# Optimization experiments

Measured on AMD Instinct MI355X. Metric: run time of the kernel, lower is better.

## Reference

```python
import jax, jax.numpy as jnp
import numpy as np

B, N, D = 4, 4096, 1024
H, S, R = 16, 256, 2           # heads, segment size, dilation rate
DH = D // H
LN_EPS = 1e-5


def _hilbert_perm(n_side):
    # perm[d] = linear index (y*side + x) of the d-th point on the Hilbert curve
    def d2xy(n, d):
        x = y = 0
        t = d
        s = 1
        while s < n:
            rx = 1 & (t // 2)
            ry = 1 & (t ^ rx)
            if ry == 0:
                if rx == 1:
                    x = s - 1 - x
                    y = s - 1 - y
                x, y = y, x
            x += s * rx
            y += s * ry
            t //= 4
            s *= 2
        return x, y
    perm = np.empty(n_side * n_side, dtype=np.int32)
    for d in range(n_side * n_side):
        xx, yy = d2xy(n_side, d)
        perm[d] = yy * n_side + xx
    return perm


def setup_inputs() -> dict:
    key = jax.random.key(0)
    ks = jax.random.split(key, 8)
    sc = 0.02
    return {
        "x": jax.random.normal(ks[0], (B, N, D), jnp.float32),
        "ln1_g": jnp.ones((D,), jnp.float32),
        "ln1_b": jnp.zeros((D,), jnp.float32),
        "w_qkv": jax.random.normal(ks[1], (D, 3 * D), jnp.float32) * sc,
        "b_qkv": jnp.zeros((3 * D,), jnp.float32),
        "w_o": jax.random.normal(ks[2], (D, D), jnp.float32) * sc,
        "b_o": jnp.zeros((D,), jnp.float32),
        "ln2_g": jnp.ones((D,), jnp.float32),
        "ln2_b": jnp.zeros((D,), jnp.float32),
        "w1": jax.random.normal(ks[3], (D, 4 * D), jnp.float32) * sc,
        "b1": jnp.zeros((4 * D,), jnp.float32),
        "w2": jax.random.normal(ks[4], (4 * D, D), jnp.float32) * sc,
        "b2": jnp.zeros((D,), jnp.float32),
        "hilbert_perm": jnp.asarray(_hilbert_perm(int(np.sqrt(N)))),
    }


def _layernorm(x, g, b):
    mu = jnp.mean(x, axis=-1, keepdims=True)
    var = jnp.mean(jnp.square(x - mu), axis=-1, keepdims=True)
    return (x - mu) * jax.lax.rsqrt(var + LN_EPS) * g + b


def _hilbert_dilated_attention(x, w_qkv, b_qkv, w_o, b_o, perm):
    b, n, d = x.shape
    nseg, sr = n // S, S // R
    xp = jnp.take(x, perm, axis=1)                    # Hilbert reorder
    qkv = xp @ w_qkv + b_qkv                          # [b,n,3d]
    q, k, v = jnp.split(qkv, 3, axis=-1)
    def seg(t):
        return t.reshape(b, nseg, S, H, DH)
    q, k, v = seg(q), seg(k), seg(v)
    # per-head dilation offset: head h attends positions (h % R) :: R in each segment
    offs = jnp.arange(H, dtype=jnp.int32) % R                        # [H]
    idx = offs[None, :] + R * jnp.arange(sr, dtype=jnp.int32)[:, None]  # [sr,H]
    idx_g = idx[None, None, :, :, None]                              # [1,1,sr,H,1]
    qd = jnp.take_along_axis(q, idx_g, axis=2)        # [b,nseg,sr,H,dh]
    kd = jnp.take_along_axis(k, idx_g, axis=2)
    vd = jnp.take_along_axis(v, idx_g, axis=2)
    scores = jnp.einsum('bgqhd,bgkhd->bghqk', qd, kd) / jnp.sqrt(jnp.asarray(DH, x.dtype))
    attn = jax.nn.softmax(scores, axis=-1)
    od = jnp.einsum('bghqk,bgkhd->bgqhd', attn, vd)   # [b,nseg,sr,H,dh]
    # scatter back into full segments; uncovered (head,pos) slots stay zero
    out = jnp.zeros((b, nseg, S, H, DH), x.dtype)
    out = out.at[:, :, idx, jnp.arange(H)[None, :], :].set(od)
    out = out.reshape(b, n, d) @ w_o + b_o
    inv = jnp.argsort(perm)
    return jnp.take(out, inv, axis=1)                 # inverse Hilbert reorder


def reference(x, ln1_g, ln1_b, w_qkv, b_qkv, w_o, b_o, ln2_g, ln2_b, w1, b1, w2, b2, hilbert_perm):
    h = _layernorm(x, ln1_g, ln1_b)
    h = _hilbert_dilated_attention(h, w_qkv, b_qkv, w_o, b_o, hilbert_perm)
    x = x + h
    h = _layernorm(x, ln2_g, ln2_b)
    h = jax.nn.gelu(h @ w1 + b1, approximate=False) @ w2 + b2
    return x + h
```

## Files before the change

kernel.cpp:

```cpp
#include <hip/hip_runtime.h>

typedef short bf16x8 __attribute__((ext_vector_type(8)));
typedef float f32x4 __attribute__((ext_vector_type(4)));
typedef unsigned short u16;

#define GLDS16(g, l) __builtin_amdgcn_global_load_lds( \
    (const __attribute__((address_space(1))) void*)(g), \
    (__attribute__((address_space(3))) void*)(l), 16, 0, 0)

#define DSR_(dst, p) asm volatile("ds_read_b128 %0, %1" \
    : "=v"(dst) : "v"((const __attribute__((address_space(3))) void*)(p)))

__device__ __forceinline__ u16 f2b(float f) {
  unsigned u = __float_as_uint(f);
  u += 0x7fffu + ((u >> 16) & 1u);
  return (u16)(u >> 16);
}

__global__ __launch_bounds__(256)
void transpose_bf16(const float* __restrict__ w, u16* __restrict__ wt, int K, int N) {
  __shared__ float tile[32][33];
  const int n0 = blockIdx.x * 32, k0 = blockIdx.y * 32;
  const int tx = threadIdx.x & 31, ty = threadIdx.x >> 5;
#pragma unroll
  for (int i = 0; i < 4; ++i)
    tile[ty + i * 8][tx] = w[(size_t)(k0 + ty + i * 8) * N + n0 + tx];
  __syncthreads();
#pragma unroll
  for (int i = 0; i < 4; ++i)
    wt[(size_t)(n0 + ty + i * 8) * K + k0 + tx] = f2b(tile[tx][ty + i * 8]);
}

__global__ __launch_bounds__(256)
void transpose_qkv_pack(const float* __restrict__ w, u16* __restrict__ wp) {
  __shared__ float tile[32][33];
  const int n0 = blockIdx.x * 32, k0 = blockIdx.y * 32;
  const int tx = threadIdx.x & 31, ty = threadIdx.x >> 5;
#pragma unroll
  for (int i = 0; i < 4; ++i)
    tile[ty + i * 8][tx] = w[(size_t)(k0 + ty + i * 8) * 3072 + n0 + tx];
  __syncthreads();
#pragma unroll
  for (int i = 0; i < 4; ++i) {
    const int col = n0 + ty + i * 8;
    const int q = (col >> 6) & 1;
    const int np = (col >> 10) * 512 + ((col >> 7) & 7) * 64 + (col & 63);
    wp[(size_t)q * (1536 * 1024) + (size_t)np * 1024 + k0 + tx] = f2b(tile[tx][ty + i * 8]);
  }
}

__global__ __launch_bounds__(256)
void transpose_wo_pack(const float* __restrict__ w, u16* __restrict__ wp) {
  __shared__ float tile[32][33];
  const int n0 = blockIdx.x * 32, k0 = blockIdx.y * 32;
  const int tx = threadIdx.x & 31, ty = threadIdx.x >> 5;
#pragma unroll
  for (int i = 0; i < 4; ++i)
    tile[ty + i * 8][tx] = w[(size_t)(k0 + ty + i * 8) * 1024 + n0 + tx];
  __syncthreads();
#pragma unroll
  for (int i = 0; i < 4; ++i) {
    const int n = n0 + ty + i * 8;
    const int k = k0 + tx;
    const int q = (k >> 6) & 1;
    const int kp = (k >> 7) * 64 + (k & 63);
    wp[(size_t)q * (1024 * 512) + (size_t)n * 512 + kp] = f2b(tile[tx][ty + i * 8]);
  }
}

__global__ __launch_bounds__(256)
void ln_rows(const float* __restrict__ src, const float* __restrict__ gam,
             const float* __restrict__ bet, const int* __restrict__ perm,
             u16* __restrict__ dst) {
  const int orow = blockIdx.x;
  const int b = orow >> 12, j = orow & 4095;
  const int srow = perm ? ((b << 12) + perm[j]) : orow;
  const float4 v = ((const float4*)(src + (size_t)srow * 1024))[threadIdx.x];
  float s = v.x + v.y + v.z + v.w;
  float s2 = v.x * v.x + v.y * v.y + v.z * v.z + v.w * v.w;
#pragma unroll
  for (int d = 1; d < 64; d <<= 1) { s += __shfl_xor(s, d); s2 += __shfl_xor(s2, d); }
  __shared__ float rs[4], rs2[4];
  const int wave = threadIdx.x >> 6, lane = threadIdx.x & 63;
  if (lane == 0) { rs[wave] = s; rs2[wave] = s2; }
  __syncthreads();
  s = rs[0] + rs[1] + rs[2] + rs[3];
  s2 = rs2[0] + rs2[1] + rs2[2] + rs2[3];
  const float mu = s * (1.f / 1024.f);
  const float var = s2 * (1.f / 1024.f) - mu * mu;
  const float rstd = rsqrtf(var + 1e-5f);
  const int c = threadIdx.x * 4;
  const float4 gg = *(const float4*)(gam + c);
  const float4 bb = *(const float4*)(bet + c);
  const u16 o0 = f2b((v.x - mu) * rstd * gg.x + bb.x);
  const u16 o1 = f2b((v.y - mu) * rstd * gg.y + bb.y);
  const u16 o2 = f2b((v.z - mu) * rstd * gg.z + bb.z);
  const u16 o3 = f2b((v.w - mu) * rstd * gg.w + bb.w);
  const unsigned lo = (unsigned)o0 | ((unsigned)o1 << 16);
  const unsigned hi = (unsigned)o2 | ((unsigned)o3 << 16);
  *(uint2*)(dst + (size_t)orow * 1024 + c) = make_uint2(lo, hi);
}

template <int EPI, int PAR>
__global__ __launch_bounds__(512, 2)
void gemm256(const u16* __restrict__ A, const u16* __restrict__ Bt,
             const float* __restrict__ bias, void* __restrict__ Cout,
             const float* __restrict__ resid, const int* __restrict__ perm,
             int M, int Nn, int K, int aRS,
             long aParOff, long bParOff, long cParOff) {
  __shared__ u16 sm[65536];
  char* const smc = (char*)sm;
  const int tid = threadIdx.x;
  const int w = tid >> 6, lane = tid & 63;
  const int lr = lane & 15, lg = lane >> 4;
  const int wm = w >> 2, wn = w & 3;

  int wg = blockIdx.x;
  int par = 0;
  if (PAR) { par = wg & 1; wg >>= 1; }
  const int x = wg & 7, l = wg >> 3;
  const int band = (M >> 8) >> 3;
  const int mm = l % band, nn = l / band;
  const int m0 = (x * band + mm) << 8;
  const int n0 = nn << 8;

  const int srow = tid >> 3;
  const int scol = ((tid & 7) ^ (srow & 7)) << 3;
  const size_t aSrc = (size_t)(m0 + srow) * aRS + (PAR ? (size_t)par * aParOff : 0) + scol;
  const size_t bSrc = (size_t)(n0 + srow) * K + (PAR ? (size_t)par * bParOff : 0) + scol;
  char* const lWav = smc + w * 1024;

  const int slot0 = (lg ^ (lr & 7)) << 4;
  const int aRow = (wm * 128 + lr) * 128;
  const int bRow = (wn * 64 + lr) * 128 + 32768;

  const int NT = K >> 6;

#define STAGE_(d, mat, h, k0) do { \
    const size_t rs_ = (mat) ? (size_t)K : (size_t)aRS; \
    const u16* gp = ((mat) ? Bt : A) + ((mat) ? bSrc : aSrc) + (size_t)(h) * 128 * rs_ + (k0); \
    char* lp = lWav + (d) * 65536 + (mat) * 32768 + (h) * 16384; \
    GLDS16(gp, lp); GLDS16(gp + 64 * rs_, lp + 8192); } while (0)

  bf16x8 aLo[8], aHi[8], bLo[4], bHi[4];

#define R_ALO(P) do { _Pragma("unroll") for (int mf = 0; mf < 4; ++mf) \
    _Pragma("unroll") for (int kk = 0; kk < 2; ++kk) \
      DSR_(aLo[mf * 2 + kk], (P) + mf * 2048 + (slot0 ^ (kk << 6))); } while (0)
#define R_AHI(P) do { _Pragma("unroll") for (int mf = 0; mf < 4; ++mf) \
    _Pragma("unroll") for (int kk = 0; kk < 2; ++kk) \
      DSR_(aHi[mf * 2 + kk], (P) + (4 + mf) * 2048 + (slot0 ^ (kk << 6))); } while (0)
#define R_BLO(P) do { _Pragma("unroll") for (int nf = 0; nf < 2; ++nf) \
    _Pragma("unroll") for (int kk = 0; kk < 2; ++kk) \
      DSR_(bLo[nf * 2 + kk], (P) + nf * 2048 + (slot0 ^ (kk << 6))); } while (0)
#define R_BHI(P) do { _Pragma("unroll") for (int nf = 0; nf < 2; ++nf) \
    _Pragma("unroll") for (int kk = 0; kk < 2; ++kk) \
      DSR_(bHi[nf * 2 + kk], (P) + (2 + nf) * 2048 + (slot0 ^ (kk << 6))); } while (0)

#define QUAD_(AARR, BARR, MB, NB) do { _Pragma("unroll") for (int mf = 0; mf < 4; ++mf) \
    _Pragma("unroll") for (int nf = 0; nf < 2; ++nf) \
    _Pragma("unroll") for (int kk = 0; kk < 2; ++kk) \
      acc[(MB) * 4 + mf][(NB) * 2 + nf] = __builtin_amdgcn_mfma_f32_16x16x32_bf16( \
          AARR[mf * 2 + kk], BARR[nf * 2 + kk], acc[(MB) * 4 + mf][(NB) * 2 + nf], 0, 0, 0); } while (0)

#define LGKM0SB_() do { asm volatile("s_waitcnt lgkmcnt(0)" ::: "memory"); \
                        __builtin_amdgcn_sched_barrier(0); } while (0)

  STAGE_(0, 1, 0, 0); STAGE_(0, 1, 1, 0); STAGE_(0, 0, 0, 0); STAGE_(0, 0, 1, 0);
  if (NT > 1) {
    STAGE_(1, 1, 0, 64); STAGE_(1, 1, 1, 64); STAGE_(1, 0, 0, 64); STAGE_(1, 0, 1, 64);
    asm volatile("s_waitcnt vmcnt(8)" ::: "memory");
  } else {
    asm volatile("s_waitcnt vmcnt(0)" ::: "memory");
  }
  __builtin_amdgcn_s_barrier();

  f32x4 acc[8][4] = {};

  for (int t = 0; t < NT; ++t) {
    const int c = t & 1;
    const char* cA = smc + c * 65536 + aRow;
    const char* cB = smc + c * 65536 + bRow;
    const int k2 = (t + 2) << 6;

    R_ALO(cA); R_BLO(cB);
    LGKM0SB_();
    __builtin_amdgcn_s_setprio(1);
    QUAD_(aLo, bLo, 0, 0);
    __builtin_amdgcn_s_setprio(0);
    R_BHI(cB);
    LGKM0SB_();
    __builtin_amdgcn_s_setprio(1);
    QUAD_(aLo, bHi, 0, 1);
    __builtin_amdgcn_s_setprio(0);
    __builtin_amdgcn_s_barrier();

    if (t + 2 < NT) { STAGE_(c, 1, 0, k2); STAGE_(c, 1, 1, k2); }
    R_AHI(cA);
    LGKM0SB_();
    __builtin_amdgcn_s_setprio(1);
    QUAD_(aHi, bLo, 1, 0);
    __builtin_amdgcn_s_setprio(0);
    __builtin_amdgcn_s_barrier();

    if (t + 2 < NT) { STAGE_(c, 0, 0, k2); STAGE_(c, 0, 1, k2); }
    __builtin_amdgcn_s_setprio(1);
    QUAD_(aHi, bHi, 1, 1);
    __builtin_amdgcn_s_setprio(0);
    if (t < NT - 2) asm volatile("s_waitcnt vmcnt(8)" ::: "memory");
    else            asm volatile("s_waitcnt vmcnt(0)" ::: "memory");
    __builtin_amdgcn_s_barrier();
  }
#undef STAGE_
#undef R_ALO
#undef R_AHI
#undef R_BLO
#undef R_BHI
#undef QUAD_
#undef LGKM0SB_

#pragma unroll
  for (int mf = 0; mf < 8; ++mf) {
#pragma unroll
    for (int nf = 0; nf < 4; ++nf) {
      const int col = n0 + wn * 64 + nf * 16 + lr;
      float bia;
      if (PAR && EPI == 0) {
        const int s = col >> 9, hh2 = (col >> 6) & 7, d = col & 63;
        bia = bias[s * 1024 + hh2 * 128 + par * 64 + d];
      } else {
        bia = bias[col];
      }
#pragma unroll
      for (int r = 0; r < 4; ++r) {
        const int row = m0 + wm * 128 + mf * 16 + lg * 4 + r;
        float v = acc[mf][nf][r] + bia;
        if (EPI == 0) {
          ((u16*)Cout)[(PAR ? (size_t)par * cParOff : 0) + (size_t)row * Nn + col] = f2b(v);
        } else if (EPI == 1) {
          v = 0.5f * v * (1.f + erff(v * 0.70710678118654752f));
          ((u16*)Cout)[(size_t)row * Nn + col] = f2b(v);
        } else if (EPI == 2) {
          const int orig = PAR ? (2 * row + par) : row;
          const int b2 = orig >> 12, jj = orig & 4095;
          const size_t di = ((size_t)((b2 << 12) + perm[jj])) * 1024 + col;
          ((float*)Cout)[di] = resid[di] + v;
        } else {
          const size_t di = (size_t)row * 1024 + col;
          ((float*)Cout)[di] = resid[di] + v;
        }
      }
    }
  }
}

__global__ __launch_bounds__(256, 2)
void attn_kernel(const u16* __restrict__ qkvp, u16* __restrict__ op) {
  const int blk = blockIdx.x;
  const int h = blk & 15, g = (blk >> 4) & 15, b = blk >> 8;
  const int tid = threadIdx.x, wave = tid >> 6, lane = tid & 63;
  const int lr = lane & 15, lg = lane >> 4;
  const int par = h & 1, hh = h >> 1;

  __shared__ u16 lQ[128 * 64];
  __shared__ u16 lK[128 * 64];
  __shared__ u16 lVt[64 * 128];
  __shared__ u16 lP[4][32 * 128];

  const u16* qp = qkvp + (size_t)par * (8192 * 1536);
  u16* opb = op + (size_t)par * (8192 * 512);
  const int rbase = (b << 11) + (g << 7);

#pragma unroll
  for (int i = 0; i < 4; ++i) {
    const int ou = i * 4096 + wave * 1024;
    const int o = ou + lane * 16;
    const int j = o >> 7, cb = o & 127;
    const u16* gq = qp + (size_t)(rbase + j) * 1536 + hh * 64 + (cb >> 1);
    GLDS16(gq, (char*)lQ + ou);
    GLDS16(gq + 512, (char*)lK + ou);
  }
#pragma unroll
  for (int i = 0; i < 4; ++i) {
    const int c = tid + i * 256;
    const int j = c >> 3, dc = c & 7;
    const uint4 vv = *(const uint4*)(qp + (size_t)(rbase + j) * 1536 + 1024 + hh * 64 + dc * 8);
    const u16* pv = (const u16*)&vv;
#pragma unroll
    for (int e = 0; e < 8; ++e) lVt[(dc * 8 + e) * 128 + j] = pv[e];
  }
  __syncthreads();

  f32x4 sacc[2][8] = {};
#pragma unroll
  for (int kk = 0; kk < 2; ++kk) {
    bf16x8 aq[2], bk[8];
#pragma unroll
    for (int mf = 0; mf < 2; ++mf)
      aq[mf] = *(const bf16x8*)&lQ[(wave * 32 + mf * 16 + lr) * 64 + kk * 32 + lg * 8];
#pragma unroll
    for (int nf = 0; nf < 8; ++nf)
      bk[nf] = *(const bf16x8*)&lK[(nf * 16 + lr) * 64 + kk * 32 + lg * 8];
#pragma unroll
    for (int mf = 0; mf < 2; ++mf)
#pragma unroll
      for (int nf = 0; nf < 8; ++nf)
        sacc[mf][nf] = __builtin_amdgcn_mfma_f32_16x16x32_bf16(aq[mf], bk[nf], sacc[mf][nf], 0, 0, 0);
  }

#pragma unroll
  for (int mf = 0; mf < 2; ++mf) {
#pragma unroll
    for (int r = 0; r < 4; ++r) {
      float mx = -3e38f;
#pragma unroll
      for (int nf = 0; nf < 8; ++nf) mx = fmaxf(mx, sacc[mf][nf][r]);
#pragma unroll
      for (int d = 1; d < 16; d <<= 1) mx = fmaxf(mx, __shfl_xor(mx, d));
      float pv[8];
      float sum = 0.f;
#pragma unroll
      for (int nf = 0; nf < 8; ++nf) {
        pv[nf] = __expf((sacc[mf][nf][r] - mx) * 0.125f);
        sum += pv[nf];
      }
#pragma unroll
      for (int d = 1; d < 16; d <<= 1) sum += __shfl_xor(sum, d);
      const float inv = 1.f / sum;
      const int rrow = mf * 16 + lg * 4 + r;
#pragma unroll
      for (int nf = 0; nf < 8; ++nf)
        lP[wave][rrow * 128 + nf * 16 + lr] = f2b(pv[nf] * inv);
    }
  }
  __syncthreads();

  f32x4 oacc[2][4] = {};
#pragma unroll
  for (int kk = 0; kk < 4; ++kk) {
    bf16x8 ap[2], bv[4];
#pragma unroll
    for (int mf = 0; mf < 2; ++mf)
      ap[mf] = *(const bf16x8*)&lP[wave][(mf * 16 + lr) * 128 + kk * 32 + lg * 8];
#pragma unroll
    for (int nf = 0; nf < 4; ++nf)
      bv[nf] = *(const bf16x8*)&lVt[(nf * 16 + lr) * 128 + kk * 32 + lg * 8];
#pragma unroll
    for (int mf = 0; mf < 2; ++mf)
#pragma unroll
      for (int nf = 0; nf < 4; ++nf)
        oacc[mf][nf] = __builtin_amdgcn_mfma_f32_16x16x32_bf16(ap[mf], bv[nf], oacc[mf][nf], 0, 0, 0);
  }

  u16* obase = opb + (size_t)rbase * 512 + hh * 64;
#pragma unroll
  for (int mf = 0; mf < 2; ++mf)
#pragma unroll
    for (int nf = 0; nf < 4; ++nf)
#pragma unroll
      for (int r = 0; r < 4; ++r) {
        const int jq = wave * 32 + mf * 16 + lg * 4 + r;
        obase[(size_t)jq * 512 + nf * 16 + lr] = f2b(oacc[mf][nf][r]);
      }
}

extern "C" void kernel_launch(void* const* d_in, const int* in_sizes, int n_in,
                              void* d_out, int out_size, void* d_ws, size_t ws_size,
                              hipStream_t stream) {
  const float* x    = (const float*)d_in[0];
  const float* ln1g = (const float*)d_in[1];
  const float* ln1b = (const float*)d_in[2];
  const float* wqkv = (const float*)d_in[3];
  const float* bqkv = (const float*)d_in[4];
  const float* wo   = (const float*)d_in[5];
  const float* bo   = (const float*)d_in[6];
  const float* ln2g = (const float*)d_in[7];
  const float* ln2b = (const float*)d_in[8];
  const float* w1   = (const float*)d_in[9];
  const float* b1   = (const float*)d_in[10];
  const float* w2   = (const float*)d_in[11];
  const float* b2   = (const float*)d_in[12];
  const int*   perm = (const int*)d_in[13];
  float* out = (float*)d_out;
  char* ws = (char*)d_ws;

  u16*  r0    = (u16*)ws;
  u16*  qkvp  = (u16*)(ws + (32ull << 20));
  u16*  op    = (u16*)(ws + (80ull << 20));
  u16*  a1    = (u16*)(ws + (32ull << 20));
  float* x2   = (float*)(ws + (160ull << 20));
  u16*  wqkvP = (u16*)(ws + (224ull << 20));
  u16*  woP   = (u16*)(ws + (230ull << 20));
  u16*  w1T   = (u16*)(ws + (232ull << 20));
  u16*  w2T   = (u16*)(ws + (240ull << 20));

  transpose_qkv_pack<<<dim3(96, 32), 256, 0, stream>>>(wqkv, wqkvP);
  transpose_wo_pack<<<dim3(32, 32), 256, 0, stream>>>(wo, woP);
  transpose_bf16<<<dim3(4096 / 32, 1024 / 32), 256, 0, stream>>>(w1, w1T, 1024, 4096);
  transpose_bf16<<<dim3(1024 / 32, 4096 / 32), 256, 0, stream>>>(w2, w2T, 4096, 1024);

  ln_rows<<<16384, 256, 0, stream>>>(x, ln1g, ln1b, perm, r0);
  gemm256<0, 1><<<384, 512, 0, stream>>>(r0, wqkvP, bqkv, qkvp, nullptr, nullptr,
                                         8192, 1536, 1024, 2048,
                                         1024L, 1536L * 1024, 8192L * 1536);
  attn_kernel<<<1024, 256, 0, stream>>>(qkvp, op);
  gemm256<2, 1><<<256, 512, 0, stream>>>(op, woP, bo, x2, x, perm,
                                         8192, 1024, 512, 512,
                                         8192L * 512, 1024L * 512, 0);
  ln_rows<<<16384, 256, 0, stream>>>(x2, ln2g, ln2b, nullptr, r0);
  gemm256<1, 0><<<1024, 512, 0, stream>>>(r0, w1T, b1, a1, nullptr, nullptr,
                                          16384, 4096, 1024, 1024, 0, 0, 0);
  gemm256<3, 0><<<256, 512, 0, stream>>>(a1, w2T, b2, out, x2, nullptr,
                                         16384, 1024, 4096, 4096, 0, 0, 0);
}
```

Before: 531.2 us.

## Switch GEMM to 256x128 tiles with triple-buffered LDS pipeline

The GEMM tile shrinks from 256x256 to 256x128, doubling the grid for every projection. The ping-pong double buffer with staged half-tile loads and four barriers per k-step becomes a three-slot ring buffer: each step loads all of A and B fragments, issues the next-next prefetch, then runs a single MFMA block with one barrier. The aim is fewer barriers per step, more workgroups to fill the CUs, and fewer accumulator registers. The cost is lower arithmetic intensity per tile, with more A reloads from global memory, and less overlap between LDS reads and MFMA work.

Measured after the change: 572.7 us. 1.08x slower.

```diff
diff --git a/kernel.cpp b/kernel.cpp
--- a/kernel.cpp
+++ b/kernel.cpp
@@ -108,7 +108,7 @@
              const float* __restrict__ resid, const int* __restrict__ perm,
              int M, int Nn, int K, int aRS,
              long aParOff, long bParOff, long cParOff) {
-  __shared__ u16 sm[65536];
+  __shared__ u16 sm[3 * 24576];
   char* const smc = (char*)sm;
   const int tid = threadIdx.x;
   const int w = tid >> 6, lane = tid & 63;
@@ -122,108 +122,80 @@
   const int band = (M >> 8) >> 3;
   const int mm = l % band, nn = l / band;
   const int m0 = (x * band + mm) << 8;
-  const int n0 = nn << 8;
+  const int n0 = nn << 7;
 
   const int srow = tid >> 3;
   const int scol = ((tid & 7) ^ (srow & 7)) << 3;
   const size_t aSrc = (size_t)(m0 + srow) * aRS + (PAR ? (size_t)par * aParOff : 0) + scol;
   const size_t bSrc = (size_t)(n0 + srow) * K + (PAR ? (size_t)par * bParOff : 0) + scol;
-  char* const lWav = smc + w * 1024;
 
   const int slot0 = (lg ^ (lr & 7)) << 4;
   const int aRow = (wm * 128 + lr) * 128;
-  const int bRow = (wn * 64 + lr) * 128 + 32768;
+  const int bRow = 32768 + (wn * 32 + lr) * 128;
 
   const int NT = K >> 6;
 
-#define STAGE_(d, mat, h, k0) do { \
-    const size_t rs_ = (mat) ? (size_t)K : (size_t)aRS; \
-    const u16* gp = ((mat) ? Bt : A) + ((mat) ? bSrc : aSrc) + (size_t)(h) * 128 * rs_ + (k0); \
-    char* lp = lWav + (d) * 65536 + (mat) * 32768 + (h) * 16384; \
-    GLDS16(gp, lp); GLDS16(gp + 64 * rs_, lp + 8192); } while (0)
-
-  bf16x8 aLo[8], aHi[8], bLo[4], bHi[4];
-
-#define R_ALO(P) do { _Pragma("unroll") for (int mf = 0; mf < 4; ++mf) \
+#define STAGE_T(d, k0) do { \
+    _Pragma("unroll") for (int i = 0; i < 4; ++i) \
+      GLDS16(A + aSrc + (size_t)(64 * i) * aRS + (k0), smc + (d) * 49152 + w * 1024 + i * 8192); \
+    _Pragma("unroll") for (int i = 0; i < 2; ++i) \
+      GLDS16(Bt + bSrc + (size_t)(64 * i) * K + (k0), smc + (d) * 49152 + 32768 + w * 1024 + i * 8192); \
+  } while (0)
+
+  bf16x8 a[16], b[4];
+
+#define R_A(P) do { _Pragma("unroll") for (int mf = 0; mf < 8; ++mf) \
     _Pragma("unroll") for (int kk = 0; kk < 2; ++kk) \
-      DSR_(aLo[mf * 2 + kk], (P) + mf * 2048 + (slot0 ^ (kk << 6))); } while (0)
-#define R_AHI(P) do { _Pragma("unroll") for (int mf = 0; mf < 4; ++mf) \
+      DSR_(a[mf * 2 + kk], (P) + mf * 2048 + (slot0 ^ (kk << 6))); } while (0)
+#define R_B(P) do { _Pragma("unroll") for (int nf = 0; nf < 2; ++nf) \
     _Pragma("unroll") for (int kk = 0; kk < 2; ++kk) \
-      DSR_(aHi[mf * 2 + kk], (P) + (4 + mf) * 2048 + (slot0 ^ (kk << 6))); } while (0)
-#define R_BLO(P) do { _Pragma("unroll") for (int nf = 0; nf < 2; ++nf) \
-    _Pragma("unroll") for (int kk = 0; kk < 2; ++kk) \
-      DSR_(bLo[nf * 2 + kk], (P) + nf * 2048 + (slot0 ^ (kk << 6))); } while (0)
-#define R_BHI(P) do { _Pragma("unroll") for (int nf = 0; nf < 2; ++nf) \
-    _Pragma("unroll") for (int kk = 0; kk < 2; ++kk) \
-      DSR_(bHi[nf * 2 + kk], (P) + (2 + nf) * 2048 + (slot0 ^ (kk << 6))); } while (0)
-
-#define QUAD_(AARR, BARR, MB, NB) do { _Pragma("unroll") for (int mf = 0; mf < 4; ++mf) \
-    _Pragma("unroll") for (int nf = 0; nf < 2; ++nf) \
-    _Pragma("unroll") for (int kk = 0; kk < 2; ++kk) \
-      acc[(MB) * 4 + mf][(NB) * 2 + nf] = __builtin_amdgcn_mfma_f32_16x16x32_bf16( \
-          AARR[mf * 2 + kk], BARR[nf * 2 + kk], acc[(MB) * 4 + mf][(NB) * 2 + nf], 0, 0, 0); } while (0)
+      DSR_(b[nf * 2 + kk], (P) + nf * 2048 + (slot0 ^ (kk << 6))); } while (0)
 
 #define LGKM0SB_() do { asm volatile("s_waitcnt lgkmcnt(0)" ::: "memory"); \
                         __builtin_amdgcn_sched_barrier(0); } while (0)
 
-  STAGE_(0, 1, 0, 0); STAGE_(0, 1, 1, 0); STAGE_(0, 0, 0, 0); STAGE_(0, 0, 1, 0);
-  if (NT > 1) {
-    STAGE_(1, 1, 0, 64); STAGE_(1, 1, 1, 64); STAGE_(1, 0, 0, 64); STAGE_(1, 0, 1, 64);
-    asm volatile("s_waitcnt vmcnt(8)" ::: "memory");
-  } else {
-    asm volatile("s_waitcnt vmcnt(0)" ::: "memory");
-  }
+  STAGE_T(0, 0);
+  if (NT > 1) { STAGE_T(1, 64); asm volatile("s_waitcnt vmcnt(6)" ::: "memory"); }
+  else        { asm volatile("s_waitcnt vmcnt(0)" ::: "memory"); }
   __builtin_amdgcn_s_barrier();
 
-  f32x4 acc[8][4] = {};
-
+  f32x4 acc[8][2] = {};
+
+  int cur = 0;
   for (int t = 0; t < NT; ++t) {
-    const int c = t & 1;
-    const char* cA = smc + c * 65536 + aRow;
-    const char* cB = smc + c * 65536 + bRow;
-    const int k2 = (t + 2) << 6;
-
-    R_ALO(cA); R_BLO(cB);
+    const char* base = smc + cur * 49152;
+    R_A(base + aRow);
+    R_B(base + bRow);
+    if (t + 2 < NT) {
+      int d = cur + 2; if (d >= 3) d -= 3;
+      STAGE_T(d, (t + 2) << 6);
+    }
     LGKM0SB_();
     __builtin_amdgcn_s_setprio(1);
-    QUAD_(aLo, bLo, 0, 0);
+#pragma unroll
+    for (int mf = 0; mf < 8; ++mf)
+#pragma unroll
+      for (int nf = 0; nf < 2; ++nf)
+#pragma unroll
+        for (int kk = 0; kk < 2; ++kk)
+          acc[mf][nf] = __builtin_amdgcn_mfma_f32_16x16x32_bf16(
+              a[mf * 2 + kk], b[nf * 2 + kk], acc[mf][nf], 0, 0, 0);
     __builtin_amdgcn_s_setprio(0);
-    R_BHI(cB);
-    LGKM0SB_();
-    __builtin_amdgcn_s_setprio(1);
-    QUAD_(aLo, bHi, 0, 1);
-    __builtin_amdgcn_s_setprio(0);
-    __builtin_amdgcn_s_barrier();
-
-    if (t + 2 < NT) { STAGE_(c, 1, 0, k2); STAGE_(c, 1, 1, k2); }
-    R_AHI(cA);
-    LGKM0SB_();
-    __builtin_amdgcn_s_setprio(1);
-    QUAD_(aHi, bLo, 1, 0);
-    __builtin_amdgcn_s_setprio(0);
-    __builtin_amdgcn_s_barrier();
-
-    if (t + 2 < NT) { STAGE_(c, 0, 0, k2); STAGE_(c, 0, 1, k2); }
-    __builtin_amdgcn_s_setprio(1);
-    QUAD_(aHi, bHi, 1, 1);
-    __builtin_amdgcn_s_setprio(0);
-    if (t < NT - 2) asm volatile("s_waitcnt vmcnt(8)" ::: "memory");
+    if (t + 2 < NT) asm volatile("s_waitcnt vmcnt(6)" ::: "memory");
     else            asm volatile("s_waitcnt vmcnt(0)" ::: "memory");
     __builtin_amdgcn_s_barrier();
-  }
-#undef STAGE_
-#undef R_ALO
-#undef R_AHI
-#undef R_BLO
-#undef R_BHI
-#undef QUAD_
+    cur = (cur + 1 == 3) ? 0 : cur + 1;
+  }
+#undef STAGE_T
+#undef R_A
+#undef R_B
 #undef LGKM0SB_
 
 #pragma unroll
   for (int mf = 0; mf < 8; ++mf) {
 #pragma unroll
-    for (int nf = 0; nf < 4; ++nf) {
-      const int col = n0 + wn * 64 + nf * 16 + lr;
+    for (int nf = 0; nf < 2; ++nf) {
+      const int col = n0 + wn * 32 + nf * 16 + lr;
       float bia;
       if (PAR && EPI == 0) {
         const int s = col >> 9, hh2 = (col >> 6) & 7, d = col & 63;
@@ -400,16 +372,16 @@
   transpose_bf16<<<dim3(1024 / 32, 4096 / 32), 256, 0, stream>>>(w2, w2T, 4096, 1024);
 
   ln_rows<<<16384, 256, 0, stream>>>(x, ln1g, ln1b, perm, r0);
-  gemm256<0, 1><<<384, 512, 0, stream>>>(r0, wqkvP, bqkv, qkvp, nullptr, nullptr,
+  gemm256<0, 1><<<768, 512, 0, stream>>>(r0, wqkvP, bqkv, qkvp, nullptr, nullptr,
                                          8192, 1536, 1024, 2048,
                                          1024L, 1536L * 1024, 8192L * 1536);
   attn_kernel<<<1024, 256, 0, stream>>>(qkvp, op);
-  gemm256<2, 1><<<256, 512, 0, stream>>>(op, woP, bo, x2, x, perm,
+  gemm256<2, 1><<<512, 512, 0, stream>>>(op, woP, bo, x2, x, perm,
                                          8192, 1024, 512, 512,
                                          8192L * 512, 1024L * 512, 0);
   ln_rows<<<16384, 256, 0, stream>>>(x2, ln2g, ln2b, nullptr, r0);
-  gemm256<1, 0><<<1024, 512, 0, stream>>>(r0, w1T, b1, a1, nullptr, nullptr,
+  gemm256<1, 0><<<2048, 512, 0, stream>>>(r0, w1T, b1, a1, nullptr, nullptr,
                                           16384, 4096, 1024, 1024, 0, 0, 0);
-  gemm256<3, 0><<<256, 512, 0, stream>>>(a1, w2T, b2, out, x2, nullptr,
+  gemm256<3, 0><<<512, 512, 0, stream>>>(a1, w2T, b2, out, x2, nullptr,
                                          16384, 1024, 4096, 4096, 0, 0, 0);
 }
```
